# Kernel optimization log

Hardware: AMD Instinct MI355X
Metric: run time of the kernel (lower is better)

## Reference

```python
import jax, jax.numpy as jnp
import numpy as np

N_MICS = 8
REF_MIC = 0
DIAG_LOAD = 1e-5
PI_ITERS = 30  # power-iteration steps for principal eigenvector of Phi_nn^-1 Phi_ss


def setup_inputs() -> dict:
    key = jax.random.key(0)
    k1, k2, k3, k4 = jax.random.split(key, 4)
    B, M, F, T = 8, N_MICS, 257, 2000
    return {
        "spec_re": jax.random.normal(k1, (B, M, F, T), dtype=jnp.float32),
        "spec_im": jax.random.normal(k2, (B, M, F, T), dtype=jnp.float32),
        "speech_mask": jax.random.uniform(k3, (B, F, T), dtype=jnp.float32),
        "noise_mask": jax.random.uniform(k4, (B, F, T), dtype=jnp.float32),
    }


def _mvdr(spec_re, spec_im, speech_mask, noise_mask):
    # (B, M, F, T) complex STFT -> (B, F, M, T) for per-(batch, freq) processing
    Y = (spec_re + 1j * spec_im).astype(jnp.complex64)
    Y = jnp.transpose(Y, (0, 2, 1, 3))  # (B, F, M, T)
    M = Y.shape[2]

    def masked_cov(mask):  # mask: (B, F, T) real
        msum = mask.sum(-1) + 1e-8                       # (B, F)
        Yw = Y * mask[:, :, None, :]                      # (B, F, M, T)
        Phi = jnp.einsum('bfmt,bfnt->bfmn', Yw, Y.conj())  # (B, F, M, M)
        return Phi / msum[..., None, None]

    Phi_ss = masked_cov(speech_mask)
    eye = jnp.eye(M, dtype=jnp.complex64)
    Phi_nn = masked_cov(noise_mask) + DIAG_LOAD * eye

    Phi_nn_inv = jnp.linalg.inv(Phi_nn)                   # batched (B, F, M, M)
    G = jnp.einsum('bfmn,bfnk->bfmk', Phi_nn_inv, Phi_ss)

    # Principal eigenvector of G via power iteration (G has real, nonnegative
    # eigenvalues since it is similar to a Hermitian-PSD generalized pencil),
    # matching torch.linalg.eig + argmax(eigenvalues.real) up to scale.
    v = jnp.ones(G.shape[:-1], dtype=jnp.complex64)       # (B, F, M)
    for _ in range(PI_ITERS):
        v = jnp.einsum('bfmn,bfn->bfm', G, v)
        v = v / (jnp.linalg.norm(v, axis=-1, keepdims=True) + 1e-12)

    # Relative transfer function normalized to reference mic (removes scale)
    rtf = v / (v[..., REF_MIC:REF_MIC + 1] + 1e-8)        # (B, F, M)

    d = jnp.einsum('bfmn,bfn->bfm', Phi_nn_inv, rtf)      # Phi_nn^-1 rtf
    denom = jnp.einsum('bfm,bfm->bf', rtf.conj(), d).real + 1e-8
    w = d / denom[..., None]                              # (B, F, M) MVDR weights

    enhanced = jnp.einsum('bfm,bfmt->bft', w.conj(), Y)   # (B, F, T) complex
    return enhanced


def reference(spec_re, spec_im, speech_mask, noise_mask):
    return _mvdr(spec_re, spec_im, speech_mask, noise_mask)
```

## Files before the change

### kernel.cpp

```cpp
#include <hip/hip_runtime.h>

#define B_DIM 8
#define M_MICS 8
#define F_DIM 257
#define T_DIM 2000

#define UP(m,n) ((m)*8 - (m)*((m)+1)/2 + (n))
#define UPI(m,n) (UP(m,n) - (m) - 1)

#define NACC 144
#define NCHUNK 9

__launch_bounds__(256, 2)
__global__ void mvdr_kernel(const float* __restrict__ sre, const float* __restrict__ sim,
                            const float* __restrict__ smask, const float* __restrict__ nmask,
                            float* __restrict__ out, int out_mode)
{
    const int f = blockIdx.x;
    const int b = blockIdx.y;
    const int tid = threadIdx.x;

    __shared__ float sred[256 * 20];
    __shared__ float spart[16 * 17];
    __shared__ float sPhi[NACC];
    __shared__ float sW[16];

    const size_t mrow = (size_t)F_DIM * T_DIM;
    const size_t base_bf = ((size_t)(b * M_MICS) * F_DIM + f) * T_DIM;
    const size_t mbase = ((size_t)b * F_DIM + f) * T_DIM;

    float acc[NACC];
#pragma unroll
    for (int i = 0; i < NACC; ++i) acc[i] = 0.f;

    for (int g = 0; g < 4; ++g) {
        const int t0 = g * 512 + 2 * tid;
        if (t0 < T_DIM) {
            float yr[M_MICS][2], yi[M_MICS][2];
#pragma unroll
            for (int m = 0; m < M_MICS; ++m) {
                const float2 vr = *reinterpret_cast<const float2*>(sre + base_bf + (size_t)m * mrow + t0);
                const float2 vi = *reinterpret_cast<const float2*>(sim + base_bf + (size_t)m * mrow + t0);
                yr[m][0] = vr.x; yr[m][1] = vr.y;
                yi[m][0] = vi.x; yi[m][1] = vi.y;
            }
            const float2 ms2 = *reinterpret_cast<const float2*>(smask + mbase + t0);
            const float2 mn2 = *reinterpret_cast<const float2*>(nmask + mbase + t0);
            const float msv[2] = { ms2.x, ms2.y };
            const float mnv[2] = { mn2.x, mn2.y };
#pragma unroll
            for (int u = 0; u < 2; ++u) {
                acc[128] += msv[u];
                acc[129] += mnv[u];
#pragma unroll
                for (int m = 0; m < M_MICS; ++m) {
                    const float pd = yr[m][u] * yr[m][u] + yi[m][u] * yi[m][u];
                    acc[UP(m, m)]      += msv[u] * pd;
                    acc[64 + UP(m, m)] += mnv[u] * pd;
#pragma unroll
                    for (int n = m + 1; n < M_MICS; ++n) {
                        const float pr = yr[m][u] * yr[n][u] + yi[m][u] * yi[n][u];
                        const float pi = yi[m][u] * yr[n][u] - yr[m][u] * yi[n][u];
                        acc[UP(m, n)]        += msv[u] * pr;
                        acc[36 + UPI(m, n)]  += msv[u] * pi;
                        acc[64 + UP(m, n)]   += mnv[u] * pr;
                        acc[100 + UPI(m, n)] += mnv[u] * pi;
                    }
                }
            }
        }
    }

#pragma unroll
    for (int c = 0; c < NCHUNK; ++c) {
        float4* dst = reinterpret_cast<float4*>(&sred[tid * 20]);
#pragma unroll
        for (int q = 0; q < 4; ++q) {
            dst[q] = make_float4(acc[c * 16 + q * 4 + 0], acc[c * 16 + q * 4 + 1],
                                 acc[c * 16 + q * 4 + 2], acc[c * 16 + q * 4 + 3]);
        }
        __syncthreads();
        {
            const int col = tid & 15, grp = tid >> 4;
            float v = 0.f;
#pragma unroll
            for (int rr = 0; rr < 16; ++rr) v += sred[(grp * 16 + rr) * 20 + col];
            spart[grp * 17 + col] = v;
        }
        __syncthreads();
        if (tid < 16) {
            float v = 0.f;
#pragma unroll
            for (int gp = 0; gp < 16; ++gp) v += spart[gp * 17 + tid];
            sPhi[c * 16 + tid] = v;
        }
        __syncthreads();
    }

    if (tid < 64) {
        const int lane = tid;
        const int r = lane >> 3, cc = lane & 7;
        const float Ssum = sPhi[128] + 1e-8f;
        const float Nsum = sPhi[129] + 1e-8f;
        const int mm = (r < cc) ? r : cc;
        const int nn2 = (r < cc) ? cc : r;
        const int P = mm * 8 - mm * (mm + 1) / 2 + nn2;
        const float sgn = (r <= cc) ? 1.f : -1.f;

        const float ssr = sPhi[P] / Ssum;
        const float ssi = (r == cc) ? 0.f : sgn * sPhi[36 + P - mm - 1] / Ssum;
        float ar = sPhi[64 + P] / Nsum + ((r == cc) ? 1e-5f : 0.f);
        float ai = (r == cc) ? 0.f : sgn * sPhi[100 + P - mm - 1] / Nsum;

        float br = (r == cc) ? 1.f : 0.f, bi = 0.f;
        for (int k = 0; k < 8; ++k) {
            const float pr = __shfl(ar, k * 9, 64);
            const float pi = __shfl(ai, k * 9, 64);
            const float den = pr * pr + pi * pi;
            const float qr = pr / den, qi = -pi / den;
            const bool isk = (r == k);
            const float ar2 = ar * qr - ai * qi;
            const float ai2 = ar * qi + ai * qr;
            const float br2 = br * qr - bi * qi;
            const float bi2 = br * qi + bi * qr;
            ar = isk ? ar2 : ar; ai = isk ? ai2 : ai;
            br = isk ? br2 : br; bi = isk ? bi2 : bi;
            const float rar = __shfl(ar, k * 8 + cc, 64);
            const float rai = __shfl(ai, k * 8 + cc, 64);
            const float rbr = __shfl(br, k * 8 + cc, 64);
            const float rbi = __shfl(bi, k * 8 + cc, 64);
            const float fr = __shfl(ar, r * 8 + k, 64);
            const float fi = __shfl(ai, r * 8 + k, 64);
            const float uar = ar - (fr * rar - fi * rai);
            const float uai = ai - (fr * rai + fi * rar);
            const float ubr = br - (fr * rbr - fi * rbi);
            const float ubi = bi - (fr * rbi + fi * rbr);
            ar = isk ? ar : uar; ai = isk ? ai : uai;
            br = isk ? br : ubr; bi = isk ? bi : ubi;
        }

        float gr = 0.f, gi = 0.f;
        for (int k = 0; k < 8; ++k) {
            const float ir = __shfl(br, r * 8 + k, 64);
            const float ii = __shfl(bi, r * 8 + k, 64);
            const float skr = __shfl(ssr, k * 8 + cc, 64);
            const float ski = __shfl(ssi, k * 8 + cc, 64);
            gr += ir * skr - ii * ski;
            gi += ir * ski + ii * skr;
        }

        float vr = 1.f, vi = 0.f;
        for (int it = 0; it < 30; ++it) {
            float wr2 = gr * vr - gi * vi;
            float wi2 = gr * vi + gi * vr;
            wr2 += __shfl_xor(wr2, 1, 64); wi2 += __shfl_xor(wi2, 1, 64);
            wr2 += __shfl_xor(wr2, 2, 64); wi2 += __shfl_xor(wi2, 2, 64);
            wr2 += __shfl_xor(wr2, 4, 64); wi2 += __shfl_xor(wi2, 4, 64);
            float nrm = wr2 * wr2 + wi2 * wi2;
            nrm += __shfl_xor(nrm, 8, 64);
            nrm += __shfl_xor(nrm, 16, 64);
            nrm += __shfl_xor(nrm, 32, 64);
            const float inv = 1.f / (sqrtf(nrm) + 1e-12f);
            wr2 *= inv; wi2 *= inv;
            vr = __shfl(wr2, cc * 9, 64);
            vi = __shfl(wi2, cc * 9, 64);
        }

        const float v0r = __shfl(vr, 0, 64) + 1e-8f;
        const float v0i = __shfl(vi, 0, 64);
        const float dd = v0r * v0r + v0i * v0i;
        const float rtr = (vr * v0r + vi * v0i) / dd;
        const float rti = (vi * v0r - vr * v0i) / dd;

        float dr = br * rtr - bi * rti;
        float di = br * rti + bi * rtr;
        dr += __shfl_xor(dr, 1, 64); di += __shfl_xor(di, 1, 64);
        dr += __shfl_xor(dr, 2, 64); di += __shfl_xor(di, 2, 64);
        dr += __shfl_xor(dr, 4, 64); di += __shfl_xor(di, 4, 64);

        float q = (r == cc) ? (rtr * dr + rti * di) : 0.f;
        q += __shfl_xor(q, 1, 64); q += __shfl_xor(q, 2, 64); q += __shfl_xor(q, 4, 64);
        q += __shfl_xor(q, 8, 64); q += __shfl_xor(q, 16, 64); q += __shfl_xor(q, 32, 64);
        q += 1e-8f;

        if (cc == 0) {
            sW[r]     = dr / q;
            sW[8 + r] = di / q;
        }
    }
    __syncthreads();

    float wr[M_MICS], wi[M_MICS];
#pragma unroll
    for (int m = 0; m < M_MICS; ++m) { wr[m] = sW[m]; wi[m] = sW[8 + m]; }

    for (int g = 0; g < 4; ++g) {
        const int t0 = g * 512 + 2 * tid;
        if (t0 < T_DIM) {
            float er0 = 0.f, ei0 = 0.f, er1 = 0.f, ei1 = 0.f;
#pragma unroll
            for (int m = 0; m < M_MICS; ++m) {
                const float2 vr2 = *reinterpret_cast<const float2*>(sre + base_bf + (size_t)m * mrow + t0);
                const float2 vi2 = *reinterpret_cast<const float2*>(sim + base_bf + (size_t)m * mrow + t0);
                er0 += wr[m] * vr2.x + wi[m] * vi2.x;
                ei0 += wr[m] * vi2.x - wi[m] * vr2.x;
                er1 += wr[m] * vr2.y + wi[m] * vi2.y;
                ei1 += wr[m] * vi2.y - wi[m] * vr2.y;
            }
            if (out_mode == 2) {
                *reinterpret_cast<float4*>(out + 2 * (mbase + t0)) = make_float4(er0, ei0, er1, ei1);
            } else {
                *reinterpret_cast<float2*>(out + mbase + t0) = make_float2(er0, er1);
            }
        }
    }
}

extern "C" void kernel_launch(void* const* d_in, const int* in_sizes, int n_in,
                              void* d_out, int out_size, void* d_ws, size_t ws_size,
                              hipStream_t stream)
{
    const float* sre   = (const float*)d_in[0];
    const float* sim   = (const float*)d_in[1];
    const float* smask = (const float*)d_in[2];
    const float* nmask = (const float*)d_in[3];

    const int mode = (out_size >= 2 * B_DIM * F_DIM * T_DIM) ? 2 : 1;

    dim3 grid(F_DIM, B_DIM);
    mvdr_kernel<<<grid, 256, 0, stream>>>(sre, sim, smask, nmask, (float*)d_out, mode);
}
```

Baseline: 160.9 us.

## Split fused MVDR kernel into covariance, solve, and apply kernels

Replaces the single per-(batch,freq) fused kernel with three kernels. The first computes the masked covariances over two time halves, with the 144 accumulators split across two half-blocks to cut register pressure. The second solves the inverse and power iteration with one wavefront per problem using shuffles. The third applies the weights over many more blocks. This aims to raise occupancy and parallelism, at the cost of workspace round-trips, extra launches, and a second full read of the spectrum in the apply pass.

```diff
diff --git a/kernel.cpp b/kernel.cpp
--- a/kernel.cpp
+++ b/kernel.cpp
@@ -4,17 +4,290 @@
 #define M_MICS 8
 #define F_DIM 257
 #define T_DIM 2000
+#define NPROB (B_DIM * F_DIM)
+#define COV_STRIDE 144
+#define NCHUNKT 2
+#define COV_FLOATS (NPROB * NCHUNKT * COV_STRIDE)
+#define W_OFFSET COV_FLOATS
+#define WS_FLOATS (COV_FLOATS + NPROB * 16)
+
+__launch_bounds__(256, 4)
+__global__ void cov_kernel(const float* __restrict__ sre, const float* __restrict__ sim,
+                           const float* __restrict__ smask, const float* __restrict__ nmask,
+                           float* __restrict__ wscov)
+{
+    const int f = blockIdx.x, b = blockIdx.y, c = blockIdx.z;
+    const int tid = threadIdx.x;
+    const int h = tid >> 7;
+    const int s = tid & 127;
+
+    const size_t mrow = (size_t)F_DIM * T_DIM;
+    const size_t base_bf = ((size_t)(b * M_MICS) * F_DIM + f) * T_DIM + (size_t)c * 1000;
+    const size_t mbase   = ((size_t)b * F_DIM + f) * T_DIM + (size_t)c * 1000;
+
+    float acc[80];
+#pragma unroll
+    for (int i = 0; i < 80; ++i) acc[i] = 0.f;
+
+    for (int g = 0; g < 4; ++g) {
+        const int t0 = 2 * s + 256 * g;
+        if (t0 < 1000) {
+            const float2 ms2 = *reinterpret_cast<const float2*>(smask + mbase + t0);
+            const float2 mn2 = *reinterpret_cast<const float2*>(nmask + mbase + t0);
+            const float msv[2] = { ms2.x, ms2.y };
+            const float mnv[2] = { mn2.x, mn2.y };
+            if (h == 0) {
+                float yr[8][2], yi[8][2];
+#pragma unroll
+                for (int m = 0; m < 8; ++m) {
+                    const float2 vr = *reinterpret_cast<const float2*>(sre + base_bf + (size_t)m * mrow + t0);
+                    const float2 vi = *reinterpret_cast<const float2*>(sim + base_bf + (size_t)m * mrow + t0);
+                    yr[m][0] = vr.x; yr[m][1] = vr.y;
+                    yi[m][0] = vi.x; yi[m][1] = vi.y;
+                }
+#pragma unroll
+                for (int u = 0; u < 2; ++u) {
+                    acc[0] += msv[u];
+                    acc[1] += mnv[u];
+#pragma unroll
+                    for (int m = 0; m < 8; ++m) {
+                        const float pd = yr[m][u] * yr[m][u] + yi[m][u] * yi[m][u];
+                        acc[2 + m]  += msv[u] * pd;
+                        acc[10 + m] += mnv[u] * pd;
+                    }
+#pragma unroll
+                    for (int m = 0; m < 8; ++m) {
+#pragma unroll
+                        for (int n = m + 1; n < 8; ++n) {
+                            const int q = m * 8 - m * (m + 1) / 2 + n - m - 1;
+                            if (q < 14) {
+                                const float pr = yr[m][u] * yr[n][u] + yi[m][u] * yi[n][u];
+                                const float pi = yi[m][u] * yr[n][u] - yr[m][u] * yi[n][u];
+                                acc[18 + 4 * q + 0] += msv[u] * pr;
+                                acc[18 + 4 * q + 1] += msv[u] * pi;
+                                acc[18 + 4 * q + 2] += mnv[u] * pr;
+                                acc[18 + 4 * q + 3] += mnv[u] * pi;
+                            }
+                        }
+                    }
+                }
+            } else {
+                float yr[6][2], yi[6][2];
+#pragma unroll
+                for (int m = 2; m < 8; ++m) {
+                    const float2 vr = *reinterpret_cast<const float2*>(sre + base_bf + (size_t)m * mrow + t0);
+                    const float2 vi = *reinterpret_cast<const float2*>(sim + base_bf + (size_t)m * mrow + t0);
+                    yr[m - 2][0] = vr.x; yr[m - 2][1] = vr.y;
+                    yi[m - 2][0] = vi.x; yi[m - 2][1] = vi.y;
+                }
+#pragma unroll
+                for (int u = 0; u < 2; ++u) {
+#pragma unroll
+                    for (int m = 2; m < 8; ++m) {
+#pragma unroll
+                        for (int n = m + 1; n < 8; ++n) {
+                            const int q = m * 8 - m * (m + 1) / 2 + n - m - 1;
+                            if (q >= 14) {
+                                const float pr = yr[m - 2][u] * yr[n - 2][u] + yi[m - 2][u] * yi[n - 2][u];
+                                const float pi = yi[m - 2][u] * yr[n - 2][u] - yr[m - 2][u] * yi[n - 2][u];
+                                acc[4 * (q - 14) + 0] += msv[u] * pr;
+                                acc[4 * (q - 14) + 1] += msv[u] * pi;
+                                acc[4 * (q - 14) + 2] += mnv[u] * pr;
+                                acc[4 * (q - 14) + 3] += mnv[u] * pi;
+                            }
+                        }
+                    }
+                }
+            }
+        }
+    }
+
+    __shared__ float sred[2][128][17];
+    __shared__ float spart[2][8][17];
+    __shared__ float sout[2][80];
+#pragma unroll
+    for (int chunk = 0; chunk < 5; ++chunk) {
+#pragma unroll
+        for (int i = 0; i < 16; ++i) sred[h][s][i] = acc[chunk * 16 + i];
+        __syncthreads();
+        {
+            const int col = s & 15, grp = s >> 4;
+            float v = 0.f;
+#pragma unroll
+            for (int rr = 0; rr < 16; ++rr) v += sred[h][grp * 16 + rr][col];
+            spart[h][grp][col] = v;
+        }
+        __syncthreads();
+        if (s < 16) {
+            float v = 0.f;
+#pragma unroll
+            for (int gp = 0; gp < 8; ++gp) v += spart[h][gp][s];
+            sout[h][chunk * 16 + s] = v;
+        }
+        __syncthreads();
+    }
+
+    const size_t wbase = ((size_t)(b * F_DIM + f) * NCHUNKT + c) * COV_STRIDE;
+    if (tid < 80)       wscov[wbase + tid] = sout[0][tid];
+    else if (tid < 144) wscov[wbase + tid] = sout[1][tid - 80];
+}
+
+__launch_bounds__(256, 4)
+__global__ void solve_kernel(const float* __restrict__ wscov, float* __restrict__ wsw)
+{
+    const int tid = threadIdx.x;
+    const int w = tid >> 6, lane = tid & 63;
+    const int p = blockIdx.x * 4 + w;
+
+    __shared__ float sPhi[4][144];
+    const size_t cb = (size_t)p * (NCHUNKT * COV_STRIDE);
+    for (int i = lane; i < 144; i += 64)
+        sPhi[w][i] = wscov[cb + i] + wscov[cb + COV_STRIDE + i];
+    __syncthreads();
+
+    const int r = lane >> 3, cc = lane & 7;
+    const float Ssum = sPhi[w][0] + 1e-8f;
+    const float Nsum = sPhi[w][1] + 1e-8f;
+
+    float ssr, ssi, ar, ai;
+    if (r == cc) {
+        ssr = sPhi[w][2 + r] / Ssum;  ssi = 0.f;
+        ar  = sPhi[w][10 + r] / Nsum + 1e-5f;  ai = 0.f;
+    } else {
+        const int mm = (r < cc) ? r : cc;
+        const int nn2 = (r < cc) ? cc : r;
+        const int q = mm * 8 - mm * (mm + 1) / 2 + nn2 - mm - 1;
+        const int basei = (q < 14) ? (18 + 4 * q) : (80 + 4 * (q - 14));
+        const float sgn = (r < cc) ? 1.f : -1.f;
+        ssr = sPhi[w][basei] / Ssum;
+        ssi = sgn * sPhi[w][basei + 1] / Ssum;
+        ar  = sPhi[w][basei + 2] / Nsum;
+        ai  = sgn * sPhi[w][basei + 3] / Nsum;
+    }
+
+    float br = (r == cc) ? 1.f : 0.f, bi = 0.f;
+    for (int k = 0; k < 8; ++k) {
+        const float pr = __shfl(ar, k * 9, 64);
+        const float pi = __shfl(ai, k * 9, 64);
+        const float den = pr * pr + pi * pi;
+        const float qr = pr / den, qi = -pi / den;
+        const bool isk = (r == k);
+        const float ar2 = ar * qr - ai * qi;
+        const float ai2 = ar * qi + ai * qr;
+        const float br2 = br * qr - bi * qi;
+        const float bi2 = br * qi + bi * qr;
+        ar = isk ? ar2 : ar; ai = isk ? ai2 : ai;
+        br = isk ? br2 : br; bi = isk ? bi2 : bi;
+        const float rar = __shfl(ar, k * 8 + cc, 64);
+        const float rai = __shfl(ai, k * 8 + cc, 64);
+        const float rbr = __shfl(br, k * 8 + cc, 64);
+        const float rbi = __shfl(bi, k * 8 + cc, 64);
+        const float fr = __shfl(ar, r * 8 + k, 64);
+        const float fi = __shfl(ai, r * 8 + k, 64);
+        const float uar = ar - (fr * rar - fi * rai);
+        const float uai = ai - (fr * rai + fi * rar);
+        const float ubr = br - (fr * rbr - fi * rbi);
+        const float ubi = bi - (fr * rbi + fi * rbr);
+        ar = isk ? ar : uar; ai = isk ? ai : uai;
+        br = isk ? br : ubr; bi = isk ? bi : ubi;
+    }
+
+    float gr = 0.f, gi = 0.f;
+    for (int k = 0; k < 8; ++k) {
+        const float ir = __shfl(br, r * 8 + k, 64);
+        const float ii = __shfl(bi, r * 8 + k, 64);
+        const float skr = __shfl(ssr, k * 8 + cc, 64);
+        const float ski = __shfl(ssi, k * 8 + cc, 64);
+        gr += ir * skr - ii * ski;
+        gi += ir * ski + ii * skr;
+    }
+
+    float vr = 1.f, vi = 0.f;
+    for (int it = 0; it < 30; ++it) {
+        float wr2 = gr * vr - gi * vi;
+        float wi2 = gr * vi + gi * vr;
+        wr2 += __shfl_xor(wr2, 1, 64); wi2 += __shfl_xor(wi2, 1, 64);
+        wr2 += __shfl_xor(wr2, 2, 64); wi2 += __shfl_xor(wi2, 2, 64);
+        wr2 += __shfl_xor(wr2, 4, 64); wi2 += __shfl_xor(wi2, 4, 64);
+        float nrm = wr2 * wr2 + wi2 * wi2;
+        nrm += __shfl_xor(nrm, 8, 64);
+        nrm += __shfl_xor(nrm, 16, 64);
+        nrm += __shfl_xor(nrm, 32, 64);
+        const float inv = 1.f / (sqrtf(nrm) + 1e-12f);
+        wr2 *= inv; wi2 *= inv;
+        vr = __shfl(wr2, cc * 9, 64);
+        vi = __shfl(wi2, cc * 9, 64);
+    }
+
+    const float v0r = __shfl(vr, 0, 64) + 1e-8f;
+    const float v0i = __shfl(vi, 0, 64);
+    const float dd = v0r * v0r + v0i * v0i;
+    const float rtr = (vr * v0r + vi * v0i) / dd;
+    const float rti = (vi * v0r - vr * v0i) / dd;
+
+    float dr = br * rtr - bi * rti;
+    float di = br * rti + bi * rtr;
+    dr += __shfl_xor(dr, 1, 64); di += __shfl_xor(di, 1, 64);
+    dr += __shfl_xor(dr, 2, 64); di += __shfl_xor(di, 2, 64);
+    dr += __shfl_xor(dr, 4, 64); di += __shfl_xor(di, 4, 64);
+
+    float qden = (r == cc) ? (rtr * dr + rti * di) : 0.f;
+    qden += __shfl_xor(qden, 1, 64); qden += __shfl_xor(qden, 2, 64);
+    qden += __shfl_xor(qden, 4, 64); qden += __shfl_xor(qden, 8, 64);
+    qden += __shfl_xor(qden, 16, 64); qden += __shfl_xor(qden, 32, 64);
+    qden += 1e-8f;
+
+    if (cc == 0) {
+        wsw[p * 16 + r]     = dr / qden;
+        wsw[p * 16 + 8 + r] = di / qden;
+    }
+}
+
+__launch_bounds__(256, 8)
+__global__ void apply_kernel(const float* __restrict__ sre, const float* __restrict__ sim,
+                             const float* __restrict__ wsw, float* __restrict__ out, int out_mode)
+{
+    const int f = blockIdx.x, b = blockIdx.y, z = blockIdx.z;
+    const int tid = threadIdx.x;
+    __shared__ float sW[16];
+    const int p = b * F_DIM + f;
+    if (tid < 16) sW[tid] = wsw[p * 16 + tid];
+    __syncthreads();
+
+    const int t0 = z * 512 + 2 * tid;
+    if (t0 >= T_DIM) return;
+
+    const size_t mrow = (size_t)F_DIM * T_DIM;
+    const size_t base_bf = ((size_t)(b * M_MICS) * F_DIM + f) * T_DIM;
+    const size_t mbase   = ((size_t)b * F_DIM + f) * T_DIM;
+
+    float er0 = 0.f, ei0 = 0.f, er1 = 0.f, ei1 = 0.f;
+#pragma unroll
+    for (int m = 0; m < 8; ++m) {
+        const float2 vr2 = *reinterpret_cast<const float2*>(sre + base_bf + (size_t)m * mrow + t0);
+        const float2 vi2 = *reinterpret_cast<const float2*>(sim + base_bf + (size_t)m * mrow + t0);
+        const float wr = sW[m], wi = sW[8 + m];
+        er0 += wr * vr2.x + wi * vi2.x;
+        ei0 += wr * vi2.x - wi * vr2.x;
+        er1 += wr * vr2.y + wi * vi2.y;
+        ei1 += wr * vi2.y - wi * vr2.y;
+    }
+    if (out_mode == 2) {
+        *reinterpret_cast<float4*>(out + 2 * (mbase + t0)) = make_float4(er0, ei0, er1, ei1);
+    } else {
+        *reinterpret_cast<float2*>(out + mbase + t0) = make_float2(er0, er1);
+    }
+}
 
 #define UP(m,n) ((m)*8 - (m)*((m)+1)/2 + (n))
 #define UPI(m,n) (UP(m,n) - (m) - 1)
-
 #define NACC 144
 #define NCHUNK 9
 
 __launch_bounds__(256, 2)
-__global__ void mvdr_kernel(const float* __restrict__ sre, const float* __restrict__ sim,
-                            const float* __restrict__ smask, const float* __restrict__ nmask,
-                            float* __restrict__ out, int out_mode)
+__global__ void mvdr_fused_kernel(const float* __restrict__ sre, const float* __restrict__ sim,
+                                  const float* __restrict__ smask, const float* __restrict__ nmask,
+                                  float* __restrict__ out, int out_mode)
 {
     const int f = blockIdx.x;
     const int b = blockIdx.y;
@@ -75,9 +348,9 @@
     for (int c = 0; c < NCHUNK; ++c) {
         float4* dst = reinterpret_cast<float4*>(&sred[tid * 20]);
 #pragma unroll
-        for (int q = 0; q < 4; ++q) {
-            dst[q] = make_float4(acc[c * 16 + q * 4 + 0], acc[c * 16 + q * 4 + 1],
-                                 acc[c * 16 + q * 4 + 2], acc[c * 16 + q * 4 + 3]);
+        for (int qq = 0; qq < 4; ++qq) {
+            dst[qq] = make_float4(acc[c * 16 + qq * 4 + 0], acc[c * 16 + qq * 4 + 1],
+                                  acc[c * 16 + qq * 4 + 2], acc[c * 16 + qq * 4 + 3]);
         }
         __syncthreads();
         {
@@ -224,9 +497,16 @@
     const float* sim   = (const float*)d_in[1];
     const float* smask = (const float*)d_in[2];
     const float* nmask = (const float*)d_in[3];
+    float* out = (float*)d_out;
+    float* ws  = (float*)d_ws;
 
     const int mode = (out_size >= 2 * B_DIM * F_DIM * T_DIM) ? 2 : 1;
 
-    dim3 grid(F_DIM, B_DIM);
-    mvdr_kernel<<<grid, 256, 0, stream>>>(sre, sim, smask, nmask, (float*)d_out, mode);
+    if (ws_size >= (size_t)WS_FLOATS * sizeof(float)) {
+        cov_kernel<<<dim3(F_DIM, B_DIM, NCHUNKT), 256, 0, stream>>>(sre, sim, smask, nmask, ws);
+        solve_kernel<<<dim3(NPROB / 4), 256, 0, stream>>>(ws, ws + W_OFFSET);
+        apply_kernel<<<dim3(F_DIM, B_DIM, 4), 256, 0, stream>>>(sre, sim, ws + W_OFFSET, out, mode);
+    } else {
+        mvdr_fused_kernel<<<dim3(F_DIM, B_DIM), 256, 0, stream>>>(sre, sim, smask, nmask, out, mode);
+    }
 }
```

Result: slower. 189.0 us (+17.5%).

## Split covariance pairs across wavefronts, reduce with shuffles instead of LDS

Applied to the files above, without the earlier changes.

Each of the four wavefronts now accumulates a disjoint subset of the mic-pair covariance terms over all time samples. This cuts each thread's accumulator count from 144 to 34, which allows launch bounds of 4 blocks per CU. The multi-stage shared-memory reduction is replaced by wavefront xor-shuffle reductions and a small shared table. The trade-off is that every wavefront now loads all spectrum data for the whole T range, so global and L2 reads during accumulation rise about fourfold.

```diff
diff --git a/kernel.cpp b/kernel.cpp
--- a/kernel.cpp
+++ b/kernel.cpp
@@ -5,40 +5,43 @@
 #define F_DIM 257
 #define T_DIM 2000
 
-#define UP(m,n) ((m)*8 - (m)*((m)+1)/2 + (n))
-#define UPI(m,n) (UP(m,n) - (m) - 1)
-
-#define NACC 144
-#define NCHUNK 9
-
-__launch_bounds__(256, 2)
-__global__ void mvdr_kernel(const float* __restrict__ sre, const float* __restrict__ sim,
-                            const float* __restrict__ smask, const float* __restrict__ nmask,
-                            float* __restrict__ out, int out_mode)
+
+#define PAIR_ACC(mq, nq, k)                                             \
+    {                                                                   \
+        const float pr = yr[mq][u] * yr[nq][u] + yi[mq][u] * yi[nq][u]; \
+        const float pi = yi[mq][u] * yr[nq][u] - yr[mq][u] * yi[nq][u]; \
+        acc[(k) + 0] += msv[u] * pr;                                    \
+        acc[(k) + 1] += msv[u] * pi;                                    \
+        acc[(k) + 2] += mnv[u] * pr;                                    \
+        acc[(k) + 3] += mnv[u] * pi;                                    \
+    }
+
+__launch_bounds__(256, 4)
+__global__ void mvdr_fused(const float* __restrict__ sre, const float* __restrict__ sim,
+                           const float* __restrict__ smask, const float* __restrict__ nmask,
+                           float* __restrict__ out, int out_mode)
 {
-    const int f = blockIdx.x;
-    const int b = blockIdx.y;
-    const int tid = threadIdx.x;
-
-    __shared__ float sred[256 * 20];
-    __shared__ float spart[16 * 17];
-    __shared__ float sPhi[NACC];
+    const int f = blockIdx.x, b = blockIdx.y, tid = threadIdx.x;
+    const int h = tid >> 6, l = tid & 63;
+
+    __shared__ float sG[4][34];
     __shared__ float sW[16];
 
     const size_t mrow = (size_t)F_DIM * T_DIM;
     const size_t base_bf = ((size_t)(b * M_MICS) * F_DIM + f) * T_DIM;
-    const size_t mbase = ((size_t)b * F_DIM + f) * T_DIM;
-
-    float acc[NACC];
-#pragma unroll
-    for (int i = 0; i < NACC; ++i) acc[i] = 0.f;
-
-    for (int g = 0; g < 4; ++g) {
-        const int t0 = g * 512 + 2 * tid;
+    const size_t mbase   = ((size_t)b * F_DIM + f) * T_DIM;
+
+    float acc[34];
+#pragma unroll
+    for (int i = 0; i < 34; ++i) acc[i] = 0.f;
+
+#pragma unroll 1
+    for (int it = 0; it < 16; ++it) {
+        const int t0 = 2 * l + 128 * it;
         if (t0 < T_DIM) {
-            float yr[M_MICS][2], yi[M_MICS][2];
-#pragma unroll
-            for (int m = 0; m < M_MICS; ++m) {
+            float yr[8][2], yi[8][2];
+#pragma unroll
+            for (int m = 0; m < 8; ++m) {
                 const float2 vr = *reinterpret_cast<const float2*>(sre + base_bf + (size_t)m * mrow + t0);
                 const float2 vi = *reinterpret_cast<const float2*>(sim + base_bf + (size_t)m * mrow + t0);
                 yr[m][0] = vr.x; yr[m][1] = vr.y;
@@ -48,69 +51,78 @@
             const float2 mn2 = *reinterpret_cast<const float2*>(nmask + mbase + t0);
             const float msv[2] = { ms2.x, ms2.y };
             const float mnv[2] = { mn2.x, mn2.y };
-#pragma unroll
-            for (int u = 0; u < 2; ++u) {
-                acc[128] += msv[u];
-                acc[129] += mnv[u];
-#pragma unroll
-                for (int m = 0; m < M_MICS; ++m) {
-                    const float pd = yr[m][u] * yr[m][u] + yi[m][u] * yi[m][u];
-                    acc[UP(m, m)]      += msv[u] * pd;
-                    acc[64 + UP(m, m)] += mnv[u] * pd;
-#pragma unroll
-                    for (int n = m + 1; n < M_MICS; ++n) {
-                        const float pr = yr[m][u] * yr[n][u] + yi[m][u] * yi[n][u];
-                        const float pi = yi[m][u] * yr[n][u] - yr[m][u] * yi[n][u];
-                        acc[UP(m, n)]        += msv[u] * pr;
-                        acc[36 + UPI(m, n)]  += msv[u] * pi;
-                        acc[64 + UP(m, n)]   += mnv[u] * pr;
-                        acc[100 + UPI(m, n)] += mnv[u] * pi;
+
+            if (h == 0) {
+#pragma unroll
+                for (int u = 0; u < 2; ++u) {
+                    acc[0] += msv[u];
+                    acc[1] += mnv[u];
+#pragma unroll
+                    for (int m = 0; m < 8; ++m) {
+                        const float pd = yr[m][u] * yr[m][u] + yi[m][u] * yi[m][u];
+                        acc[2 + m]  += msv[u] * pd;
+                        acc[10 + m] += mnv[u] * pd;
                     }
-                }
-            }
-        }
-    }
-
-#pragma unroll
-    for (int c = 0; c < NCHUNK; ++c) {
-        float4* dst = reinterpret_cast<float4*>(&sred[tid * 20]);
-#pragma unroll
-        for (int q = 0; q < 4; ++q) {
-            dst[q] = make_float4(acc[c * 16 + q * 4 + 0], acc[c * 16 + q * 4 + 1],
-                                 acc[c * 16 + q * 4 + 2], acc[c * 16 + q * 4 + 3]);
-        }
-        __syncthreads();
-        {
-            const int col = tid & 15, grp = tid >> 4;
-            float v = 0.f;
-#pragma unroll
-            for (int rr = 0; rr < 16; ++rr) v += sred[(grp * 16 + rr) * 20 + col];
-            spart[grp * 17 + col] = v;
-        }
-        __syncthreads();
-        if (tid < 16) {
-            float v = 0.f;
-#pragma unroll
-            for (int gp = 0; gp < 16; ++gp) v += spart[gp * 17 + tid];
-            sPhi[c * 16 + tid] = v;
-        }
-        __syncthreads();
-    }
+                    PAIR_ACC(0, 1, 18) PAIR_ACC(0, 2, 22) PAIR_ACC(0, 3, 26) PAIR_ACC(0, 4, 30)
+                }
+            } else if (h == 1) {
+#pragma unroll
+                for (int u = 0; u < 2; ++u) {
+                    PAIR_ACC(0, 5, 0)  PAIR_ACC(0, 6, 4)  PAIR_ACC(0, 7, 8)  PAIR_ACC(1, 2, 12)
+                    PAIR_ACC(1, 3, 16) PAIR_ACC(1, 4, 20) PAIR_ACC(1, 5, 24) PAIR_ACC(1, 6, 28)
+                }
+            } else if (h == 2) {
+#pragma unroll
+                for (int u = 0; u < 2; ++u) {
+                    PAIR_ACC(1, 7, 0)  PAIR_ACC(2, 3, 4)  PAIR_ACC(2, 4, 8)  PAIR_ACC(2, 5, 12)
+                    PAIR_ACC(2, 6, 16) PAIR_ACC(2, 7, 20) PAIR_ACC(3, 4, 24) PAIR_ACC(3, 5, 28)
+                }
+            } else {
+#pragma unroll
+                for (int u = 0; u < 2; ++u) {
+                    PAIR_ACC(3, 6, 0)  PAIR_ACC(3, 7, 4)  PAIR_ACC(4, 5, 8)  PAIR_ACC(4, 6, 12)
+                    PAIR_ACC(4, 7, 16) PAIR_ACC(5, 6, 20) PAIR_ACC(5, 7, 24) PAIR_ACC(6, 7, 28)
+                }
+            }
+        }
+    }
+
+#pragma unroll
+    for (int i = 0; i < 34; ++i) {
+        acc[i] += __shfl_xor(acc[i], 1, 64);
+        acc[i] += __shfl_xor(acc[i], 2, 64);
+        acc[i] += __shfl_xor(acc[i], 4, 64);
+        acc[i] += __shfl_xor(acc[i], 8, 64);
+        acc[i] += __shfl_xor(acc[i], 16, 64);
+        acc[i] += __shfl_xor(acc[i], 32, 64);
+    }
+    if (l == 0) {
+#pragma unroll
+        for (int i = 0; i < 34; ++i) sG[h][i] = acc[i];
+    }
+    __syncthreads();
 
     if (tid < 64) {
-        const int lane = tid;
-        const int r = lane >> 3, cc = lane & 7;
-        const float Ssum = sPhi[128] + 1e-8f;
-        const float Nsum = sPhi[129] + 1e-8f;
-        const int mm = (r < cc) ? r : cc;
-        const int nn2 = (r < cc) ? cc : r;
-        const int P = mm * 8 - mm * (mm + 1) / 2 + nn2;
-        const float sgn = (r <= cc) ? 1.f : -1.f;
-
-        const float ssr = sPhi[P] / Ssum;
-        const float ssi = (r == cc) ? 0.f : sgn * sPhi[36 + P - mm - 1] / Ssum;
-        float ar = sPhi[64 + P] / Nsum + ((r == cc) ? 1e-5f : 0.f);
-        float ai = (r == cc) ? 0.f : sgn * sPhi[100 + P - mm - 1] / Nsum;
+        const int r = tid >> 3, cc = tid & 7;
+        const float Ssum = sG[0][0] + 1e-8f;
+        const float Nsum = sG[0][1] + 1e-8f;
+
+        float ssr, ssi, ar, ai;
+        if (r == cc) {
+            ssr = sG[0][2 + r] / Ssum;  ssi = 0.f;
+            ar  = sG[0][10 + r] / Nsum + 1e-5f;  ai = 0.f;
+        } else {
+            const int mm  = (r < cc) ? r : cc;
+            const int nn2 = (r < cc) ? cc : r;
+            const int q = mm * 8 - mm * (mm + 1) / 2 + nn2 - mm - 1;
+            const int g = (q < 4) ? 0 : (1 + ((q - 4) >> 3));
+            const int basei = (q < 4) ? (18 + 4 * q) : (4 * ((q - 4) & 7));
+            const float sgn = (r < cc) ? 1.f : -1.f;
+            ssr = sG[g][basei] / Ssum;
+            ssi = sgn * sG[g][basei + 1] / Ssum;
+            ar  = sG[g][basei + 2] / Nsum;
+            ai  = sgn * sG[g][basei + 3] / Nsum;
+        }
 
         float br = (r == cc) ? 1.f : 0.f, bi = 0.f;
         for (int k = 0; k < 8; ++k) {
@@ -150,7 +162,7 @@
         }
 
         float vr = 1.f, vi = 0.f;
-        for (int it = 0; it < 30; ++it) {
+        for (int itp = 0; itp < 30; ++itp) {
             float wr2 = gr * vr - gi * vi;
             float wi2 = gr * vi + gi * vr;
             wr2 += __shfl_xor(wr2, 1, 64); wi2 += __shfl_xor(wi2, 1, 64);
@@ -178,14 +190,15 @@
         dr += __shfl_xor(dr, 2, 64); di += __shfl_xor(di, 2, 64);
         dr += __shfl_xor(dr, 4, 64); di += __shfl_xor(di, 4, 64);
 
-        float q = (r == cc) ? (rtr * dr + rti * di) : 0.f;
-        q += __shfl_xor(q, 1, 64); q += __shfl_xor(q, 2, 64); q += __shfl_xor(q, 4, 64);
-        q += __shfl_xor(q, 8, 64); q += __shfl_xor(q, 16, 64); q += __shfl_xor(q, 32, 64);
-        q += 1e-8f;
+        float qden = (r == cc) ? (rtr * dr + rti * di) : 0.f;
+        qden += __shfl_xor(qden, 1, 64); qden += __shfl_xor(qden, 2, 64);
+        qden += __shfl_xor(qden, 4, 64); qden += __shfl_xor(qden, 8, 64);
+        qden += __shfl_xor(qden, 16, 64); qden += __shfl_xor(qden, 32, 64);
+        qden += 1e-8f;
 
         if (cc == 0) {
-            sW[r]     = dr / q;
-            sW[8 + r] = di / q;
+            sW[r]     = dr / qden;
+            sW[8 + r] = di / qden;
         }
     }
     __syncthreads();
@@ -194,6 +207,7 @@
 #pragma unroll
     for (int m = 0; m < M_MICS; ++m) { wr[m] = sW[m]; wi[m] = sW[8 + m]; }
 
+#pragma unroll 1
     for (int g = 0; g < 4; ++g) {
         const int t0 = g * 512 + 2 * tid;
         if (t0 < T_DIM) {
@@ -224,9 +238,9 @@
     const float* sim   = (const float*)d_in[1];
     const float* smask = (const float*)d_in[2];
     const float* nmask = (const float*)d_in[3];
+    float* out = (float*)d_out;
 
     const int mode = (out_size >= 2 * B_DIM * F_DIM * T_DIM) ? 2 : 1;
 
-    dim3 grid(F_DIM, B_DIM);
-    mvdr_kernel<<<grid, 256, 0, stream>>>(sre, sim, smask, nmask, (float*)d_out, mode);
+    mvdr_fused<<<dim3(F_DIM, B_DIM), 256, 0, stream>>>(sre, sim, smask, nmask, out, mode);
 }
```

Result: slower. 182.0 us (+13.1%).
